# Kernel optimization log

Hardware: AMD Instinct MI355X
Metric: run time of the kernel (lower is better)

Reference implementation:

```python
import jax, jax.numpy as jnp
import numpy as np

CS = [32, 32, 64, 128, 256, 256, 128, 96, 96]
NC = 19
N0, N1, N2, N3, N4 = 50000, 20000, 8000, 3200, 1300


def build_shapes():
    cs = CS
    def rb(ci, co):
        t = [(27, ci, co), (27, co, co)]
        if ci != co:
            t.append((ci, co))  # 1x1 shortcut conv
        return t
    s = [(27, 4, cs[0]), (27, cs[0], cs[0])]                       # stem
    s += [(8, cs[0], cs[0])] + rb(cs[0], cs[1]) + rb(cs[1], cs[1])  # stage1
    s += [(8, cs[1], cs[1])] + rb(cs[1], cs[2]) + rb(cs[2], cs[2])  # stage2
    s += [(8, cs[2], cs[2])] + rb(cs[2], cs[3]) + rb(cs[3], cs[3])  # stage3
    s += [(8, cs[3], cs[3])] + rb(cs[3], cs[4]) + rb(cs[4], cs[4])  # stage4
    s += [(8, cs[4], cs[5])] + rb(cs[5] + cs[3], cs[5]) + rb(cs[5], cs[5])  # up1
    s += [(8, cs[5], cs[6])] + rb(cs[6] + cs[2], cs[6]) + rb(cs[6], cs[6])  # up2
    s += [(8, cs[6], cs[7])] + rb(cs[7] + cs[1], cs[7]) + rb(cs[7], cs[7])  # up3
    s += [(8, cs[7], cs[8])] + rb(cs[8] + cs[0], cs[8]) + rb(cs[8], cs[8])  # up4
    s += [(cs[8], NC), (NC,), (cs[8], cs[8]), (cs[8],), (cs[8], 128), (128,)]
    return s

P_TOTAL = sum(int(np.prod(sh)) for sh in build_shapes())


def _bn(x):
    # train-mode BatchNorm, gamma=1 beta=0 (set by weight_initialization)
    return (x - x.mean(0)) * jax.lax.rsqrt(jnp.var(x, 0) + 1e-5)


def _spconv(x, nbr, W):
    # sparse conv as gather-GEMM-scatter over K kernel offsets.
    # x: [Nin, Cin], nbr: [Nout, K] row indices into x, W: [K, Cin, Cout]
    acc0 = jnp.zeros((nbr.shape[0], W.shape[-1]), x.dtype)
    def step(acc, kw):
        idx, Wk = kw
        return acc + x[idx] @ Wk, None
    acc, _ = jax.lax.scan(step, acc0, (nbr.T, W))
    return acc


def _spdeconv(x, parent, off, W):
    # transposed ks=2 stride=2 conv: each fine voxel has exactly one coarse
    # parent and one kernel-offset id. out[i] = x[parent[i]] @ W[off[i]]
    y = jnp.einsum('nc,kcd->nkd', x[parent], W)  # [Nf, 8, Cout]
    return jnp.take_along_axis(y, off[:, None, None], axis=1)[:, 0, :]


def _cbr(x, nbr, W):
    return jax.nn.relu(_bn(_spconv(x, nbr, W)))


def _resblock(x, nbr, take, ci, co):
    w1 = take(); w2 = take()
    h = _bn(_spconv(jax.nn.relu(_bn(_spconv(x, nbr, w1))), nbr, w2))
    s = x if ci == co else _bn(x @ take())
    return jax.nn.relu(h + s)


def _forward(x, nbr0, nbr1, nbr2, nbr3, nbr4, d1, d2, d3, d4,
             u1p, u1o, u2p, u2o, u3p, u3o, u4p, u4o, params):
    parts = []
    o = 0
    for sh in build_shapes():
        n = int(np.prod(sh))
        parts.append(params[o:o + n].reshape(sh))
        o += n
    it = iter(parts)
    take = lambda: next(it)
    cs = CS
    x0 = _cbr(x, nbr0, take()); x0 = _cbr(x0, nbr0, take())            # stem
    h = _cbr(x0, d1, take())
    h = _resblock(h, nbr1, take, cs[0], cs[1]); x1 = _resblock(h, nbr1, take, cs[1], cs[1])
    h = _cbr(x1, d2, take())
    h = _resblock(h, nbr2, take, cs[1], cs[2]); x2 = _resblock(h, nbr2, take, cs[2], cs[2])
    h = _cbr(x2, d3, take())
    h = _resblock(h, nbr3, take, cs[2], cs[3]); x3 = _resblock(h, nbr3, take, cs[3], cs[3])
    h = _cbr(x3, d4, take())
    h = _resblock(h, nbr4, take, cs[3], cs[4]); x4 = _resblock(h, nbr4, take, cs[4], cs[4])
    y = jax.nn.relu(_bn(_spdeconv(x4, u1p, u1o, take())))
    y = jnp.concatenate([y, x3], 1)
    y = _resblock(y, nbr3, take, cs[5] + cs[3], cs[5]); y = _resblock(y, nbr3, take, cs[5], cs[5])
    y = jax.nn.relu(_bn(_spdeconv(y, u2p, u2o, take())))
    y = jnp.concatenate([y, x2], 1)
    y = _resblock(y, nbr2, take, cs[6] + cs[2], cs[6]); y = _resblock(y, nbr2, take, cs[6], cs[6])
    y = jax.nn.relu(_bn(_spdeconv(y, u3p, u3o, take())))
    y = jnp.concatenate([y, x1], 1)
    y = _resblock(y, nbr1, take, cs[7] + cs[1], cs[7]); y = _resblock(y, nbr1, take, cs[7], cs[7])
    y = jax.nn.relu(_bn(_spdeconv(y, u4p, u4o, take())))
    y = jnp.concatenate([y, x0], 1)
    y = _resblock(y, nbr0, take, cs[8] + cs[0], cs[8]); y = _resblock(y, nbr0, take, cs[8], cs[8])
    wc = take(); bc = take(); w1 = take(); b1 = take(); w2 = take(); b2 = take()
    out = y @ wc + bc                             # classifier logits [N0, NC]
    feat = jax.nn.relu(y @ w1 + b1) @ w2 + b2     # projection head [N0, 128]
    return out, feat


def setup_inputs() -> dict:
    key = jax.random.key(0)
    ks = jax.random.split(key, 20)
    ri = lambda k, shape, hi: jax.random.randint(k, shape, 0, hi, dtype=jnp.int32)
    return {
        'x': jax.random.normal(ks[0], (N0, 4), jnp.float32),
        'nbr0': ri(ks[1], (N0, 27), N0), 'nbr1': ri(ks[2], (N1, 27), N1),
        'nbr2': ri(ks[3], (N2, 27), N2), 'nbr3': ri(ks[4], (N3, 27), N3),
        'nbr4': ri(ks[5], (N4, 27), N4),
        'd1': ri(ks[6], (N1, 8), N0), 'd2': ri(ks[7], (N2, 8), N1),
        'd3': ri(ks[8], (N3, 8), N2), 'd4': ri(ks[9], (N4, 8), N3),
        'u1p': ri(ks[10], (N3,), N4), 'u1o': ri(ks[11], (N3,), 8),
        'u2p': ri(ks[12], (N2,), N3), 'u2o': ri(ks[13], (N2,), 8),
        'u3p': ri(ks[14], (N1,), N2), 'u3o': ri(ks[15], (N1,), 8),
        'u4p': ri(ks[16], (N0,), N1), 'u4o': ri(ks[17], (N0,), 8),
        'params': jax.random.normal(ks[18], (P_TOTAL,), jnp.float32) * 0.05,
    }


def reference(x, nbr0, nbr1, nbr2, nbr3, nbr4, d1, d2, d3, d4,
              u1p, u1o, u2p, u2o, u3p, u3o, u4p, u4o, params):
    return _forward(x, nbr0, nbr1, nbr2, nbr3, nbr4, d1, d2, d3, d4,
                    u1p, u1o, u2p, u2o, u3p, u3o, u4p, u4o, params)
```

## Files before the change

kernel.cpp:

```cpp
#include <hip/hip_runtime.h>
#include <hip/hip_bf16.h>
#include <stdint.h>

typedef __hip_bfloat16 hbf;
typedef unsigned short u16;
typedef __attribute__((ext_vector_type(8))) short bfrag;
typedef __attribute__((ext_vector_type(4))) float f4;

#define NP0 50000
#define NP1 20000
#define NP2 8000
#define NP3 3200
#define NP4 1300

static inline int cdiv(int a, int b) { return (a + b - 1) / b; }

static __device__ __forceinline__ float u2f(u16 u) { return __uint_as_float(((unsigned)u) << 16); }
static __device__ __forceinline__ u16 f2u(float f) {
  hbf h = __float2bfloat16(f);
  u16 r; __builtin_memcpy(&r, &h, 2); return r;
}
static __device__ __forceinline__ float pload(const void* P, int isbf, size_t i) {
  return isbf ? u2f(((const u16*)P)[i]) : ((const float*)P)[i];
}

__global__ void k_sniff(const void* __restrict__ xraw, int* __restrict__ flagp) {
  __shared__ float smax[256];
  const u16* u = (const u16*)xraw;
  float m = 0.f;
  for (int i = threadIdx.x; i < 2048; i += 256) {
    float v = u2f(u[2 * i]);
    if (isnan(v) || isinf(v)) m = 1e30f; else m = fmaxf(m, fabsf(v));
  }
  smax[threadIdx.x] = m;
  __syncthreads();
  for (int s = 128; s > 0; s >>= 1) {
    if (threadIdx.x < s) smax[threadIdx.x] = fmaxf(smax[threadIdx.x], smax[threadIdx.x + s]);
    __syncthreads();
  }
  if (threadIdx.x == 0) *flagp = (smax[0] < 1e4f) ? 1 : 0;
}

__global__ __launch_bounds__(256) void k_prep_frag(
    const void* __restrict__ P, const int* __restrict__ flagp, u16* __restrict__ W,
    long src, long halfel, int K, int CI, int CO, int CB32, int NT16)
{
  int f = *flagp;
  long total = (long)K * CB32 * NT16 * 64;
  for (long c = (long)blockIdx.x * 256 + threadIdx.x; c < total; c += (long)gridDim.x * 256) {
    int lane = (int)(c & 63); long t = c >> 6;
    int nt = (int)(t % NT16); t /= NT16;
    int cb = (int)(t % CB32); int k = (int)(t / CB32);
    int co = nt * 16 + (lane & 15);
    int cib = cb * 32 + (lane >> 4) * 8;
    u16 hi[8], lo[8];
#pragma unroll
    for (int j = 0; j < 8; ++j) {
      int ci = cib + j; float v = 0.f;
      if (ci < CI && co < CO) v = pload(P, f, src + ((size_t)k * CI + ci) * CO + co);
      u16 h = f2u(v);
      hi[j] = h;
      lo[j] = f2u(v - u2f(h));
    }
    *(bfrag*)(W + c * 8) = *(const bfrag*)hi;
    *(bfrag*)(W + halfel + c * 8) = *(const bfrag*)lo;
  }
}

__global__ void k_prep_bias(const void* __restrict__ P, const int* __restrict__ flagp,
                            float* __restrict__ B, long src, int n)
{
  int f = *flagp;
  int i = blockIdx.x * 256 + threadIdx.x;
  if (i < n) B[i] = pload(P, f, src + i);
}

__global__ void k_pad(const void* __restrict__ xraw, const int* __restrict__ flagp,
                      float* __restrict__ Xp, int N)
{
  int f = *flagp; int total = N * 32;
  for (int i = blockIdx.x * 256 + threadIdx.x; i < total; i += gridDim.x * 256) {
    int n = i >> 5, cc = i & 31;
    Xp[i] = (cc < 4) ? pload(xraw, f, (size_t)n * 4 + cc) : 0.f;
  }
}

template<int NT>
__global__ __launch_bounds__(256) void k_conv_mfma(
    const float* __restrict__ X, const int* __restrict__ nbr,
    const u16* __restrict__ Wp, long halfel, float* __restrict__ Y,
    const float* __restrict__ bias, int relu,
    int N, int K, int CB32, int NT16, int CO, int XS, int tlen, int atomic)
{
  const int lane = threadIdx.x & 63;
  const int wv = threadIdx.x >> 6;
  const int rowbase = blockIdx.x * 128 + wv * 32;
  const int ntb = blockIdx.y * NT;
  const int ml = lane & 15;
  const int quad = lane >> 4;
  const int ktot = K * CB32;
  const int t0 = blockIdx.z * tlen;
  const int t1 = (t0 + tlen < ktot) ? (t0 + tlen) : ktot;

  f4 acc[2][NT];
#pragma unroll
  for (int i = 0; i < 2; ++i)
#pragma unroll
    for (int j = 0; j < NT; ++j) acc[i][j] = (f4)(0.f);

  int k = t0 / CB32;
  int cb = t0 - k * CB32;
  int idx[2];
  bool fresh = true;

  for (int t = t0; t < t1; ++t) {
    if (fresh) {
#pragma unroll
      for (int mt = 0; mt < 2; ++mt) {
        int r = rowbase + mt * 16 + ml;
        idx[mt] = (r < N) ? (nbr ? nbr[(size_t)r * K + k] : r) : 0;
      }
      fresh = false;
    }
    const u16* WH = Wp + (size_t)t * NT16 * 512;
    const u16* WL = WH + halfel;
    bfrag bh[NT], bl[NT];
#pragma unroll
    for (int nt = 0; nt < NT; ++nt) {
      size_t o = ((size_t)(ntb + nt) * 64 + lane) * 8;
      bh[nt] = *(const bfrag*)(WH + o);
      bl[nt] = *(const bfrag*)(WL + o);
    }
    bfrag ahi[2], alo[2];
#pragma unroll
    for (int mt = 0; mt < 2; ++mt) {
      const float* ap = X + (size_t)idx[mt] * XS + cb * 32 + quad * 8;
      float4 q0 = *(const float4*)ap;
      float4 q1 = *(const float4*)(ap + 4);
      float av[8] = {q0.x, q0.y, q0.z, q0.w, q1.x, q1.y, q1.z, q1.w};
      u16 hi8[8], lo8[8];
#pragma unroll
      for (int j = 0; j < 8; ++j) {
        u16 hh = f2u(av[j]);
        hi8[j] = hh;
        lo8[j] = f2u(av[j] - u2f(hh));
      }
      __builtin_memcpy(&ahi[mt], hi8, 16);
      __builtin_memcpy(&alo[mt], lo8, 16);
    }
#pragma unroll
    for (int mt = 0; mt < 2; ++mt)
#pragma unroll
      for (int nt = 0; nt < NT; ++nt) {
        acc[mt][nt] = __builtin_amdgcn_mfma_f32_16x16x32_bf16(alo[mt], bh[nt], acc[mt][nt], 0, 0, 0);
        acc[mt][nt] = __builtin_amdgcn_mfma_f32_16x16x32_bf16(ahi[mt], bl[nt], acc[mt][nt], 0, 0, 0);
        acc[mt][nt] = __builtin_amdgcn_mfma_f32_16x16x32_bf16(ahi[mt], bh[nt], acc[mt][nt], 0, 0, 0);
      }
    if (++cb == CB32) { cb = 0; ++k; fresh = true; }
  }

#pragma unroll
  for (int mt = 0; mt < 2; ++mt) {
#pragma unroll
    for (int nt = 0; nt < NT; ++nt) {
      int col = (ntb + nt) * 16 + ml;
      if (col >= CO) continue;
      float bvv = bias ? bias[col] : 0.f;
#pragma unroll
      for (int reg = 0; reg < 4; ++reg) {
        int row = rowbase + mt * 16 + quad * 4 + reg;
        if (row < N) {
          if (atomic) {
            atomicAdd(&Y[(size_t)row * CO + col], acc[mt][nt][reg]);
          } else {
            float v = acc[mt][nt][reg] + bvv;
            if (relu) v = fmaxf(v, 0.f);
            Y[(size_t)row * CO + col] = v;
          }
        }
      }
    }
  }
}

__global__ void k_bias_relu(float* __restrict__ Y, const float* __restrict__ bias,
                            int relu, int total, int CO)
{
  int stride = gridDim.x * 256;
  for (int i = blockIdx.x * 256 + threadIdx.x; i < total; i += stride) {
    int c = i % CO;
    float v = Y[i] + (bias ? bias[c] : 0.f);
    if (relu) v = fmaxf(v, 0.f);
    Y[i] = v;
  }
}

static void launch_conv(hipStream_t s, int bx, const float* X, const int* nbr,
                        const u16* W, long halfel, float* Y, const float* bias, int relu,
                        int N, int K, int CB32, int NT16, int CO, int XS)
{
  int NT = (NT16 % 6 == 0) ? 6 : ((NT16 % 4 == 0) ? 4 : 2);
  int ny = NT16 / NT;
  int ktot = K * CB32;
  long blocks = (long)bx * ny;
  int ZS = 1;
  if (ktot > 1) {
    ZS = (int)((1024 + blocks - 1) / blocks);
    if (ZS > ktot) ZS = ktot;
    if (ZS < 1) ZS = 1;
  }
  int tlen = cdiv(ktot, ZS);
  ZS = cdiv(ktot, tlen);
  int atomic = (ZS > 1) ? 1 : 0;
  if (atomic) hipMemsetAsync(Y, 0, (size_t)N * CO * 4, s);
  dim3 g(bx, ny, ZS);
  if (NT == 6)      k_conv_mfma<6><<<g, 256, 0, s>>>(X, nbr, W, halfel, Y, bias, relu, N, K, CB32, NT16, CO, XS, tlen, atomic);
  else if (NT == 4) k_conv_mfma<4><<<g, 256, 0, s>>>(X, nbr, W, halfel, Y, bias, relu, N, K, CB32, NT16, CO, XS, tlen, atomic);
  else              k_conv_mfma<2><<<g, 256, 0, s>>>(X, nbr, W, halfel, Y, bias, relu, N, K, CB32, NT16, CO, XS, tlen, atomic);
  if (atomic && (bias || relu)) {
    int total = N * CO;
    int nb = cdiv(total, 1024); if (nb > 1024) nb = 1024; if (nb < 1) nb = 1;
    k_bias_relu<<<nb, 256, 0, s>>>(Y, bias, relu, total, CO);
  }
}

__global__ __launch_bounds__(256) void k_deconv(
    const float* __restrict__ X, const int* __restrict__ par, const int* __restrict__ off,
    const void* __restrict__ P, long wofs, const int* __restrict__ flagp,
    float* __restrict__ Y, int N, int CI, int CO)
{
  int f = *flagp;
  int lane = threadIdx.x & 63, wv = threadIdx.x >> 6;
  int n = blockIdx.y * 4 + wv; if (n >= N) return;
  int co = blockIdx.x * 64 + lane; if (co >= CO) return;
  const float* xr = X + (size_t)par[n] * CI;
  size_t wbase = wofs + (size_t)off[n] * CI * CO + co;
  float acc = 0.f;
  for (int ci = 0; ci < CI; ci += 4) {
    float4 xv = *(const float4*)(xr + ci);
    acc += xv.x * pload(P, f, wbase + (size_t)ci * CO);
    acc += xv.y * pload(P, f, wbase + (size_t)(ci + 1) * CO);
    acc += xv.z * pload(P, f, wbase + (size_t)(ci + 2) * CO);
    acc += xv.w * pload(P, f, wbase + (size_t)(ci + 3) * CO);
  }
  Y[(size_t)n * CO + co] = acc;
}

__global__ __launch_bounds__(256) void k_bn_stats(
    const float* __restrict__ X, float* __restrict__ st, int total, int C)
{
  __shared__ float ssum[384], ssq[384];
  for (int c = threadIdx.x; c < C; c += 256) { ssum[c] = 0.f; ssq[c] = 0.f; }
  __syncthreads();
  int gid = blockIdx.x * 256 + threadIdx.x;
  int total4 = total >> 2;
  int stride = gridDim.x * 256;
  int c0 = (gid * 4) % C;
  float s0 = 0.f, s1 = 0.f, s2 = 0.f, s3 = 0.f;
  float q0 = 0.f, q1 = 0.f, q2 = 0.f, q3 = 0.f;
  for (int i = gid; i < total4; i += stride) {
    float4 v = ((const float4*)X)[i];
    s0 += v.x; q0 += v.x * v.x;
    s1 += v.y; q1 += v.y * v.y;
    s2 += v.z; q2 += v.z * v.z;
    s3 += v.w; q3 += v.w * v.w;
  }
  atomicAdd(&ssum[c0], s0);     atomicAdd(&ssq[c0], q0);
  atomicAdd(&ssum[c0 + 1], s1); atomicAdd(&ssq[c0 + 1], q1);
  atomicAdd(&ssum[c0 + 2], s2); atomicAdd(&ssq[c0 + 2], q2);
  atomicAdd(&ssum[c0 + 3], s3); atomicAdd(&ssq[c0 + 3], q3);
  __syncthreads();
  for (int c = threadIdx.x; c < C; c += 256) {
    atomicAdd(&st[c], ssum[c]); atomicAdd(&st[384 + c], ssq[c]);
  }
}

__global__ __launch_bounds__(256) void k_bn_apply(
    const float* __restrict__ X, const float* __restrict__ st, const float* __restrict__ add,
    float* __restrict__ Y, int relu, int total, int C, float invN)
{
  __shared__ float mean[384], rsig[384];
  for (int c = threadIdx.x; c < C; c += 256) {
    float mm = st[c] * invN;
    float vv = st[384 + c] * invN - mm * mm;
    mean[c] = mm; rsig[c] = rsqrtf(vv + 1e-5f);
  }
  __syncthreads();
  int gid = blockIdx.x * 256 + threadIdx.x;
  int total4 = total >> 2;
  int stride = gridDim.x * 256;
  int c0 = (gid * 4) % C;
  float m0 = mean[c0], m1 = mean[c0 + 1], m2 = mean[c0 + 2], m3 = mean[c0 + 3];
  float r0 = rsig[c0], r1 = rsig[c0 + 1], r2 = rsig[c0 + 2], r3 = rsig[c0 + 3];
  for (int i = gid; i < total4; i += stride) {
    float4 v = ((const float4*)X)[i];
    v.x = (v.x - m0) * r0; v.y = (v.y - m1) * r1;
    v.z = (v.z - m2) * r2; v.w = (v.w - m3) * r3;
    if (add) {
      float4 a = ((const float4*)add)[i];
      v.x += a.x; v.y += a.y; v.z += a.z; v.w += a.w;
    }
    if (relu) {
      v.x = fmaxf(v.x, 0.f); v.y = fmaxf(v.y, 0.f);
      v.z = fmaxf(v.z, 0.f); v.w = fmaxf(v.w, 0.f);
    }
    ((float4*)Y)[i] = v;
  }
}

__global__ void k_copycols(const float* __restrict__ S, float* __restrict__ D,
                           int N, int Cs, int Cd, int off)
{
  int csq = Cs >> 2;
  int total4 = N * csq;
  int stride = gridDim.x * 256;
  for (int i = blockIdx.x * 256 + threadIdx.x; i < total4; i += stride) {
    int n = i / csq, cc = i - n * csq;
    ((float4*)D)[((size_t)n * Cd + off) / 4 + cc] = ((const float4*)S)[i];
  }
}

__global__ void k_store_dyn(const float* __restrict__ S, void* __restrict__ D,
                            const int* __restrict__ flagp, size_t eofs, int n)
{
  int f = *flagp;
  int n4 = n >> 2;
  int stride = gridDim.x * 256;
  for (int i = blockIdx.x * 256 + threadIdx.x; i < n4; i += stride) {
    float4 v = ((const float4*)S)[i];
    if (f) {
      ushort4 u;
      u.x = f2u(v.x); u.y = f2u(v.y); u.z = f2u(v.z); u.w = f2u(v.w);
      *(ushort4*)((u16*)D + eofs + (size_t)i * 4) = u;
    } else {
      *(float4*)((float*)D + eofs + (size_t)i * 4) = v;
    }
  }
}


extern "C" void kernel_launch(void* const* d_in, const int* in_sizes, int n_in,
                              void* d_out, int out_size, void* d_ws, size_t ws_size,
                              hipStream_t stream)
{
  const void* xraw = d_in[0];
  const int* nbr0 = (const int*)d_in[1];
  const int* nbr1 = (const int*)d_in[2];
  const int* nbr2 = (const int*)d_in[3];
  const int* nbr3 = (const int*)d_in[4];
  const int* nbr4 = (const int*)d_in[5];
  const int* d1 = (const int*)d_in[6];
  const int* d2 = (const int*)d_in[7];
  const int* d3 = (const int*)d_in[8];
  const int* d4 = (const int*)d_in[9];
  const int* u1p = (const int*)d_in[10]; const int* u1o = (const int*)d_in[11];
  const int* u2p = (const int*)d_in[12]; const int* u2o = (const int*)d_in[13];
  const int* u3p = (const int*)d_in[14]; const int* u3o = (const int*)d_in[15];
  const int* u4p = (const int*)d_in[16]; const int* u4o = (const int*)d_in[17];
  const void* params = d_in[18];
  (void)in_sizes; (void)n_in;

  char* base = (char*)d_ws; size_t off = 0;
  auto ab = [&](size_t bytes) -> void* { void* p = base + off; off += (bytes + 63) & ~(size_t)63; return p; };
  int* flagp = (int*)ab(64);
  float* st = (float*)ab((size_t)64 * 768 * 4);
  u16* Wst = (u16*)ab((size_t)5400000 * 2);
  float* Bstf = (float*)ab((size_t)512 * 4);
  float* x0 = (float*)ab((size_t)NP0 * 32 * 4);
  float* x1 = (float*)ab((size_t)NP1 * 32 * 4);
  float* x2 = (float*)ab((size_t)NP2 * 64 * 4);
  float* x3 = (float*)ab((size_t)NP3 * 128 * 4);
  float* x4 = (float*)ab((size_t)NP4 * 256 * 4);
  float* U  = (float*)ab((size_t)NP0 * 96 * 4);
  float* A  = (float*)ab((size_t)NP0 * 96 * 4);
  float* B  = (float*)ab((size_t)NP0 * 128 * 4);
  float* Xp = B;
  if (off > ws_size) { hipMemsetAsync(d_out, 0, (size_t)out_size * 2, stream); return; }

  long po = 0;
  int bnc = 0;

  auto prepF = [&](int K, int CI, int CO, int CB32, int NT16) -> long {
    long chunks = (long)K * CB32 * NT16 * 64;
    long halfel = chunks * 8;
    int nb = (int)((chunks + 255) / 256); if (nb > 4096) nb = 4096; if (nb < 1) nb = 1;
    k_prep_frag<<<nb, 256, 0, stream>>>(params, flagp, Wst, po, halfel, K, CI, CO, CB32, NT16);
    po += (long)K * CI * CO;
    return halfel;
  };
  auto convop = [&](const float* X, const int* nb_, int K, int CI, int CO, float* Y, int N, int XS) {
    int CB32 = cdiv(CI, 32), NT16 = cdiv(CO, 16);
    long halfel = prepF(K, CI, CO, CB32, NT16);
    launch_conv(stream, cdiv(N, 128), X, nb_, Wst, halfel, Y, nullptr, 0, N, K, CB32, NT16, CO, XS);
  };
  auto linop = [&](const float* X, int CI, int CO, float* Y, int N, bool bias, int relu) {
    int CB32 = cdiv(CI, 32), NT16 = cdiv(CO, 16);
    long halfel = prepF(1, CI, CO, CB32, NT16);
    const float* bp = nullptr;
    if (bias) {
      k_prep_bias<<<cdiv(CO, 256), 256, 0, stream>>>(params, flagp, Bstf, po, CO);
      po += CO; bp = Bstf;
    }
    launch_conv(stream, cdiv(N, 128), X, nullptr, Wst, halfel, Y, bp, relu, N, 1, CB32, NT16, CO, CI);
  };
  auto deconvop = [&](const float* X, const int* par, const int* ofv, int CI, int CO, float* Y, int N) {
    long wofs = po; po += (long)8 * CI * CO;
    dim3 g(cdiv(CO, 64), cdiv(N, 4));
    k_deconv<<<g, 256, 0, stream>>>(X, par, ofv, params, wofs, flagp, Y, N, CI, CO);
  };
  auto bnop = [&](const float* X, int N, int C, const float* add, int relu, float* out) {
    float* slot = st + (size_t)(bnc++) * 768;
    int total = N * C;
    int total4 = total >> 2;
    int nb1 = cdiv(total4, 4096); if (nb1 > 504) nb1 = 504; if (nb1 < 3) nb1 = 3;
    nb1 = ((nb1 + 2) / 3) * 3;
    k_bn_stats<<<nb1, 256, 0, stream>>>(X, slot, total, C);
    int nb2 = cdiv(total4, 2048); if (nb2 > 510) nb2 = 510; if (nb2 < 3) nb2 = 3;
    nb2 = ((nb2 + 2) / 3) * 3;
    k_bn_apply<<<nb2, 256, 0, stream>>>(X, slot, add, out ? out : (float*)X, relu, total, C, 1.0f / (float)N);
  };
  auto copyop = [&](const float* S, float* D, int N, int Cs, int Cd, int o2) {
    int total4 = (N * Cs) >> 2;
    int nb3 = cdiv(total4, 1024); if (nb3 > 1024) nb3 = 1024; if (nb3 < 1) nb3 = 1;
    k_copycols<<<nb3, 256, 0, stream>>>(S, D, N, Cs, Cd, o2);
  };
  auto storeop = [&](const float* S, size_t eo, int n) {
    int nb4 = cdiv(n >> 2, 1024); if (nb4 > 1024) nb4 = 1024; if (nb4 < 1) nb4 = 1;
    k_store_dyn<<<nb4, 256, 0, stream>>>(S, d_out, flagp, eo, n);
  };
  auto resblock = [&](const int* nb, int N, int CI, int CO,
                      float* H, float* t1, float* t2, float* OUT) {
    convop(H, nb, 27, CI, CO, t1, N, CI);
    bnop(t1, N, CO, nullptr, 1, nullptr);
    convop(t1, nb, 27, CO, CO, t2, N, CO);
    const float* S;
    if (CI == CO) S = H;
    else { linop(H, CI, CO, t1, N, false, 0); bnop(t1, N, CO, nullptr, 0, nullptr); S = t1; }
    bnop(t2, N, CO, S, 1, OUT);
  };

  k_sniff<<<1, 256, 0, stream>>>(xraw, flagp);
  hipMemsetAsync(st, 0, (size_t)64 * 768 * 4, stream);
  k_pad<<<1024, 256, 0, stream>>>(xraw, flagp, Xp, NP0);

  convop(Xp, nbr0, 27, 4, 32, A, NP0, 32);  bnop(A, NP0, 32, nullptr, 1, nullptr);
  convop(A, nbr0, 27, 32, 32, x0, NP0, 32); bnop(x0, NP0, 32, nullptr, 1, nullptr);
  convop(x0, d1, 8, 32, 32, U, NP1, 32); bnop(U, NP1, 32, nullptr, 1, nullptr);
  resblock(nbr1, NP1, 32, 32, U, A, B, U);
  resblock(nbr1, NP1, 32, 32, U, A, B, x1);
  convop(x1, d2, 8, 32, 32, U, NP2, 32); bnop(U, NP2, 32, nullptr, 1, nullptr);
  resblock(nbr2, NP2, 32, 64, U, A, B, U);
  resblock(nbr2, NP2, 64, 64, U, A, B, x2);
  convop(x2, d3, 8, 64, 64, U, NP3, 64); bnop(U, NP3, 64, nullptr, 1, nullptr);
  resblock(nbr3, NP3, 64, 128, U, A, B, U);
  resblock(nbr3, NP3, 128, 128, U, A, B, x3);
  convop(x3, d4, 8, 128, 128, U, NP4, 128); bnop(U, NP4, 128, nullptr, 1, nullptr);
  resblock(nbr4, NP4, 128, 256, U, A, B, U);
  resblock(nbr4, NP4, 256, 256, U, A, B, x4);
  deconvop(x4, u1p, u1o, 256, 256, A, NP3); bnop(A, NP3, 256, nullptr, 1, nullptr);
  copyop(A, B, NP3, 256, 384, 0); copyop(x3, B, NP3, 128, 384, 256);
  resblock(nbr3, NP3, 384, 256, B, A, U, B);
  resblock(nbr3, NP3, 256, 256, B, A, U, U);
  deconvop(U, u2p, u2o, 256, 128, A, NP2); bnop(A, NP2, 128, nullptr, 1, nullptr);
  copyop(A, B, NP2, 128, 192, 0); copyop(x2, B, NP2, 64, 192, 128);
  resblock(nbr2, NP2, 192, 128, B, A, U, B);
  resblock(nbr2, NP2, 128, 128, B, A, U, U);
  deconvop(U, u3p, u3o, 128, 96, A, NP1); bnop(A, NP1, 96, nullptr, 1, nullptr);
  copyop(A, B, NP1, 96, 128, 0); copyop(x1, B, NP1, 32, 128, 96);
  resblock(nbr1, NP1, 128, 96, B, A, U, B);
  resblock(nbr1, NP1, 96, 96, B, A, U, U);
  deconvop(U, u4p, u4o, 96, 96, A, NP0); bnop(A, NP0, 96, nullptr, 1, nullptr);
  copyop(A, B, NP0, 96, 128, 0); copyop(x0, B, NP0, 32, 128, 96);
  resblock(nbr0, NP0, 128, 96, B, A, U, B);
  resblock(nbr0, NP0, 96, 96, B, A, U, U);
  linop(U, 96, 19, x0, NP0, true, 0);
  linop(U, 96, 96, A, NP0, true, 1);
  linop(A, 96, 128, B, NP0, true, 0);
  storeop(x0, 0, NP0 * 19);
  storeop(B, (size_t)NP0 * 19, NP0 * 128);
}
```

Measured before the change: 4.423 ms.

## Batch all weight fragment preparation into one kernel and skip low-half MFMA for bf16 params

Weight splitting for every conv layer is replaced by a single k_prep_all launch driven by a host-built descriptor table, writing all layers into one large workspace buffer when space allows. This removes many small per-layer prep launches. The conv kernel also reads the dtype flag, and when parameters are bf16 (low half zero) it drops the bl loads and the ahi*bl MFMA, cutting MFMA work by a third. It adds a host-to-device table copy and relies on the hand-written table matching the forward layer order.

```diff
diff --git a/kernel.cpp b/kernel.cpp
--- a/kernel.cpp
+++ b/kernel.cpp
@@ -23,6 +23,14 @@
 static __device__ __forceinline__ float pload(const void* P, int isbf, size_t i) {
   return isbf ? u2f(((const u16*)P)[i]) : ((const float*)P)[i];
 }
+
+
+struct PrepD {
+  long cpre;
+  long src;
+  long dst;
+  int K, CI, CO, CB32, NT16, pad;
+};
 
 __global__ void k_sniff(const void* __restrict__ xraw, int* __restrict__ flagp) {
   __shared__ float smax[256];
@@ -39,6 +47,35 @@
     __syncthreads();
   }
   if (threadIdx.x == 0) *flagp = (smax[0] < 1e4f) ? 1 : 0;
+}
+
+__global__ __launch_bounds__(256) void k_prep_all(
+    const void* __restrict__ P, const int* __restrict__ flagp, u16* __restrict__ W,
+    const PrepD* __restrict__ T, int NL, long totalC, long totalE)
+{
+  int f = *flagp;
+  int L = 0;
+  for (long c = (long)blockIdx.x * 256 + threadIdx.x; c < totalC; c += (long)gridDim.x * 256) {
+    while (L + 1 < NL && c >= T[L + 1].cpre) ++L;
+    PrepD d = T[L];
+    long lc = c - d.cpre;
+    int lane = (int)(lc & 63); long t = lc >> 6;
+    int nt = (int)(t % d.NT16); t /= d.NT16;
+    int cb = (int)(t % d.CB32); int k = (int)(t / d.CB32);
+    int co = nt * 16 + (lane & 15);
+    int cib = cb * 32 + (lane >> 4) * 8;
+    u16 hi[8], lo[8];
+#pragma unroll
+    for (int j = 0; j < 8; ++j) {
+      int ci = cib + j; float v = 0.f;
+      if (ci < d.CI && co < d.CO) v = pload(P, f, d.src + ((size_t)k * d.CI + ci) * d.CO + co);
+      u16 h = f2u(v);
+      hi[j] = h;
+      lo[j] = f2u(v - u2f(h));
+    }
+    *(bfrag*)(W + d.dst + lc * 8) = *(const bfrag*)hi;
+    *(bfrag*)(W + totalE + d.dst + lc * 8) = *(const bfrag*)lo;
+  }
 }
 
 __global__ __launch_bounds__(256) void k_prep_frag(
@@ -89,9 +126,10 @@
 __global__ __launch_bounds__(256) void k_conv_mfma(
     const float* __restrict__ X, const int* __restrict__ nbr,
     const u16* __restrict__ Wp, long halfel, float* __restrict__ Y,
-    const float* __restrict__ bias, int relu,
+    const float* __restrict__ bias, int relu, const int* __restrict__ flagp,
     int N, int K, int CB32, int NT16, int CO, int XS, int tlen, int atomic)
 {
+  const int f = *flagp;
   const int lane = threadIdx.x & 63;
   const int wv = threadIdx.x >> 6;
   const int rowbase = blockIdx.x * 128 + wv * 32;
@@ -113,50 +151,95 @@
   int idx[2];
   bool fresh = true;
 
-  for (int t = t0; t < t1; ++t) {
-    if (fresh) {
+  if (f) {
+    for (int t = t0; t < t1; ++t) {
+      if (fresh) {
+#pragma unroll
+        for (int mt = 0; mt < 2; ++mt) {
+          int r = rowbase + mt * 16 + ml;
+          idx[mt] = (r < N) ? (nbr ? nbr[(size_t)r * K + k] : r) : 0;
+        }
+        fresh = false;
+      }
+      const u16* WH = Wp + (size_t)t * NT16 * 512;
+      bfrag bh[NT];
+#pragma unroll
+      for (int nt = 0; nt < NT; ++nt) {
+        size_t o = ((size_t)(ntb + nt) * 64 + lane) * 8;
+        bh[nt] = *(const bfrag*)(WH + o);
+      }
+      bfrag ahi[2], alo[2];
 #pragma unroll
       for (int mt = 0; mt < 2; ++mt) {
-        int r = rowbase + mt * 16 + ml;
-        idx[mt] = (r < N) ? (nbr ? nbr[(size_t)r * K + k] : r) : 0;
+        const float* ap = X + (size_t)idx[mt] * XS + cb * 32 + quad * 8;
+        float4 q0 = *(const float4*)ap;
+        float4 q1 = *(const float4*)(ap + 4);
+        float av[8] = {q0.x, q0.y, q0.z, q0.w, q1.x, q1.y, q1.z, q1.w};
+        u16 hi8[8], lo8[8];
+#pragma unroll
+        for (int j = 0; j < 8; ++j) {
+          u16 hh = f2u(av[j]);
+          hi8[j] = hh;
+          lo8[j] = f2u(av[j] - u2f(hh));
+        }
+        __builtin_memcpy(&ahi[mt], hi8, 16);
+        __builtin_memcpy(&alo[mt], lo8, 16);
       }
-      fresh = false;
-    }
-    const u16* WH = Wp + (size_t)t * NT16 * 512;
-    const u16* WL = WH + halfel;
-    bfrag bh[NT], bl[NT];
-#pragma unroll
-    for (int nt = 0; nt < NT; ++nt) {
-      size_t o = ((size_t)(ntb + nt) * 64 + lane) * 8;
-      bh[nt] = *(const bfrag*)(WH + o);
-      bl[nt] = *(const bfrag*)(WL + o);
-    }
-    bfrag ahi[2], alo[2];
-#pragma unroll
-    for (int mt = 0; mt < 2; ++mt) {
-      const float* ap = X + (size_t)idx[mt] * XS + cb * 32 + quad * 8;
-      float4 q0 = *(const float4*)ap;
-      float4 q1 = *(const float4*)(ap + 4);
-      float av[8] = {q0.x, q0.y, q0.z, q0.w, q1.x, q1.y, q1.z, q1.w};
-      u16 hi8[8], lo8[8];
-#pragma unroll
-      for (int j = 0; j < 8; ++j) {
-        u16 hh = f2u(av[j]);
-        hi8[j] = hh;
-        lo8[j] = f2u(av[j] - u2f(hh));
+#pragma unroll
+      for (int mt = 0; mt < 2; ++mt)
+#pragma unroll
+        for (int nt = 0; nt < NT; ++nt) {
+          acc[mt][nt] = __builtin_amdgcn_mfma_f32_16x16x32_bf16(alo[mt], bh[nt], acc[mt][nt], 0, 0, 0);
+          acc[mt][nt] = __builtin_amdgcn_mfma_f32_16x16x32_bf16(ahi[mt], bh[nt], acc[mt][nt], 0, 0, 0);
+        }
+      if (++cb == CB32) { cb = 0; ++k; fresh = true; }
+    }
+  } else {
+    for (int t = t0; t < t1; ++t) {
+      if (fresh) {
+#pragma unroll
+        for (int mt = 0; mt < 2; ++mt) {
+          int r = rowbase + mt * 16 + ml;
+          idx[mt] = (r < N) ? (nbr ? nbr[(size_t)r * K + k] : r) : 0;
+        }
+        fresh = false;
       }
-      __builtin_memcpy(&ahi[mt], hi8, 16);
-      __builtin_memcpy(&alo[mt], lo8, 16);
-    }
-#pragma unroll
-    for (int mt = 0; mt < 2; ++mt)
+      const u16* WH = Wp + (size_t)t * NT16 * 512;
+      const u16* WL = WH + halfel;
+      bfrag bh[NT], bl[NT];
 #pragma unroll
       for (int nt = 0; nt < NT; ++nt) {
-        acc[mt][nt] = __builtin_amdgcn_mfma_f32_16x16x32_bf16(alo[mt], bh[nt], acc[mt][nt], 0, 0, 0);
-        acc[mt][nt] = __builtin_amdgcn_mfma_f32_16x16x32_bf16(ahi[mt], bl[nt], acc[mt][nt], 0, 0, 0);
-        acc[mt][nt] = __builtin_amdgcn_mfma_f32_16x16x32_bf16(ahi[mt], bh[nt], acc[mt][nt], 0, 0, 0);
+        size_t o = ((size_t)(ntb + nt) * 64 + lane) * 8;
+        bh[nt] = *(const bfrag*)(WH + o);
+        bl[nt] = *(const bfrag*)(WL + o);
       }
-    if (++cb == CB32) { cb = 0; ++k; fresh = true; }
+      bfrag ahi[2], alo[2];
+#pragma unroll
+      for (int mt = 0; mt < 2; ++mt) {
+        const float* ap = X + (size_t)idx[mt] * XS + cb * 32 + quad * 8;
+        float4 q0 = *(const float4*)ap;
+        float4 q1 = *(const float4*)(ap + 4);
+        float av[8] = {q0.x, q0.y, q0.z, q0.w, q1.x, q1.y, q1.z, q1.w};
+        u16 hi8[8], lo8[8];
+#pragma unroll
+        for (int j = 0; j < 8; ++j) {
+          u16 hh = f2u(av[j]);
+          hi8[j] = hh;
+          lo8[j] = f2u(av[j] - u2f(hh));
+        }
+        __builtin_memcpy(&ahi[mt], hi8, 16);
+        __builtin_memcpy(&alo[mt], lo8, 16);
+      }
+#pragma unroll
+      for (int mt = 0; mt < 2; ++mt)
+#pragma unroll
+        for (int nt = 0; nt < NT; ++nt) {
+          acc[mt][nt] = __builtin_amdgcn_mfma_f32_16x16x32_bf16(alo[mt], bh[nt], acc[mt][nt], 0, 0, 0);
+          acc[mt][nt] = __builtin_amdgcn_mfma_f32_16x16x32_bf16(ahi[mt], bl[nt], acc[mt][nt], 0, 0, 0);
+          acc[mt][nt] = __builtin_amdgcn_mfma_f32_16x16x32_bf16(ahi[mt], bh[nt], acc[mt][nt], 0, 0, 0);
+        }
+      if (++cb == CB32) { cb = 0; ++k; fresh = true; }
+    }
   }
 
 #pragma unroll
@@ -197,7 +280,7 @@
 
 static void launch_conv(hipStream_t s, int bx, const float* X, const int* nbr,
                         const u16* W, long halfel, float* Y, const float* bias, int relu,
-                        int N, int K, int CB32, int NT16, int CO, int XS)
+                        const int* flagp, int N, int K, int CB32, int NT16, int CO, int XS)
 {
   int NT = (NT16 % 6 == 0) ? 6 : ((NT16 % 4 == 0) ? 4 : 2);
   int ny = NT16 / NT;
@@ -214,9 +297,9 @@
   int atomic = (ZS > 1) ? 1 : 0;
   if (atomic) hipMemsetAsync(Y, 0, (size_t)N * CO * 4, s);
   dim3 g(bx, ny, ZS);
-  if (NT == 6)      k_conv_mfma<6><<<g, 256, 0, s>>>(X, nbr, W, halfel, Y, bias, relu, N, K, CB32, NT16, CO, XS, tlen, atomic);
-  else if (NT == 4) k_conv_mfma<4><<<g, 256, 0, s>>>(X, nbr, W, halfel, Y, bias, relu, N, K, CB32, NT16, CO, XS, tlen, atomic);
-  else              k_conv_mfma<2><<<g, 256, 0, s>>>(X, nbr, W, halfel, Y, bias, relu, N, K, CB32, NT16, CO, XS, tlen, atomic);
+  if (NT == 6)      k_conv_mfma<6><<<g, 256, 0, s>>>(X, nbr, W, halfel, Y, bias, relu, flagp, N, K, CB32, NT16, CO, XS, tlen, atomic);
+  else if (NT == 4) k_conv_mfma<4><<<g, 256, 0, s>>>(X, nbr, W, halfel, Y, bias, relu, flagp, N, K, CB32, NT16, CO, XS, tlen, atomic);
+  else              k_conv_mfma<2><<<g, 256, 0, s>>>(X, nbr, W, halfel, Y, bias, relu, flagp, N, K, CB32, NT16, CO, XS, tlen, atomic);
   if (atomic && (bias || relu)) {
     int total = N * CO;
     int nb = cdiv(total, 1024); if (nb > 1024) nb = 1024; if (nb < 1) nb = 1;
@@ -336,6 +419,34 @@
       *(float4*)((float*)D + eofs + (size_t)i * 4) = v;
     }
   }
+}
+
+static int build_table(PrepD* T, long* totalC, long* totalE) {
+  int n = 0; long po = 0, ce = 0, cc = 0;
+  auto W = [&](int K, int CI, int CO) {
+    int CB = cdiv(CI, 32), NTx = cdiv(CO, 16);
+    long ch = (long)K * CB * NTx * 64;
+    T[n].cpre = cc; T[n].src = po; T[n].dst = ce;
+    T[n].K = K; T[n].CI = CI; T[n].CO = CO; T[n].CB32 = CB; T[n].NT16 = NTx; T[n].pad = 0;
+    ++n; cc += ch; ce += ch * 8; po += (long)K * CI * CO;
+  };
+  auto SKIP = [&](long e) { po += e; };
+  W(27, 4, 32); W(27, 32, 32);
+  W(8, 32, 32); W(27, 32, 32); W(27, 32, 32); W(27, 32, 32); W(27, 32, 32);
+  W(8, 32, 32); W(27, 32, 64); W(27, 64, 64); W(1, 32, 64); W(27, 64, 64); W(27, 64, 64);
+  W(8, 64, 64); W(27, 64, 128); W(27, 128, 128); W(1, 64, 128); W(27, 128, 128); W(27, 128, 128);
+  W(8, 128, 128); W(27, 128, 256); W(27, 256, 256); W(1, 128, 256); W(27, 256, 256); W(27, 256, 256);
+  SKIP(8L * 256 * 256);
+  W(27, 384, 256); W(27, 256, 256); W(1, 384, 256); W(27, 256, 256); W(27, 256, 256);
+  SKIP(8L * 256 * 128);
+  W(27, 192, 128); W(27, 128, 128); W(1, 192, 128); W(27, 128, 128); W(27, 128, 128);
+  SKIP(8L * 128 * 96);
+  W(27, 128, 96); W(27, 96, 96); W(1, 128, 96); W(27, 96, 96); W(27, 96, 96);
+  SKIP(8L * 96 * 96);
+  W(27, 128, 96); W(27, 96, 96); W(1, 128, 96); W(27, 96, 96); W(27, 96, 96);
+  W(1, 96, 19); SKIP(19); W(1, 96, 96); SKIP(96); W(1, 96, 128); SKIP(128);
+  *totalC = cc; *totalE = ce;
+  return n;
 }
 
 
@@ -360,11 +471,14 @@
   const void* params = d_in[18];
   (void)in_sizes; (void)n_in;
 
+  static PrepD h_table[64];
+  long totalC = 0, totalE = 0;
+  int NL = build_table(h_table, &totalC, &totalE);
+
   char* base = (char*)d_ws; size_t off = 0;
   auto ab = [&](size_t bytes) -> void* { void* p = base + off; off += (bytes + 63) & ~(size_t)63; return p; };
   int* flagp = (int*)ab(64);
   float* st = (float*)ab((size_t)64 * 768 * 4);
-  u16* Wst = (u16*)ab((size_t)5400000 * 2);
   float* Bstf = (float*)ab((size_t)512 * 4);
   float* x0 = (float*)ab((size_t)NP0 * 32 * 4);
   float* x1 = (float*)ab((size_t)NP1 * 32 * 4);
@@ -375,10 +489,22 @@
   float* A  = (float*)ab((size_t)NP0 * 96 * 4);
   float* B  = (float*)ab((size_t)NP0 * 128 * 4);
   float* Xp = B;
+
+  size_t wall_bytes = (size_t)totalE * 4;
+  size_t rem = (ws_size > off) ? (ws_size - off) : 0;
+  bool bigprep = rem >= wall_bytes + 8192;
+  u16* Wall = nullptr; PrepD* d_table = nullptr; u16* Wst = nullptr;
+  if (bigprep) {
+    Wall = (u16*)ab(wall_bytes);
+    d_table = (PrepD*)ab(4096);
+  } else {
+    Wst = (u16*)ab((size_t)5400000 * 2);
+  }
   if (off > ws_size) { hipMemsetAsync(d_out, 0, (size_t)out_size * 2, stream); return; }
 
   long po = 0;
   int bnc = 0;
+  int wli = 0;
 
   auto prepF = [&](int K, int CI, int CO, int CB32, int NT16) -> long {
     long chunks = (long)K * CB32 * NT16 * 64;
@@ -388,20 +514,30 @@
     po += (long)K * CI * CO;
     return halfel;
   };
+  auto getW = [&](int K, int CI, int CO, int CB32, int NT16, const u16** Wp, long* he) {
+    if (bigprep) {
+      *Wp = Wall + h_table[wli].dst; *he = totalE;
+      ++wli; po += (long)K * CI * CO;
+    } else {
+      *he = prepF(K, CI, CO, CB32, NT16); *Wp = Wst;
+    }
+  };
   auto convop = [&](const float* X, const int* nb_, int K, int CI, int CO, float* Y, int N, int XS) {
     int CB32 = cdiv(CI, 32), NT16 = cdiv(CO, 16);
-    long halfel = prepF(K, CI, CO, CB32, NT16);
-    launch_conv(stream, cdiv(N, 128), X, nb_, Wst, halfel, Y, nullptr, 0, N, K, CB32, NT16, CO, XS);
+    const u16* Wp; long he;
+    getW(K, CI, CO, CB32, NT16, &Wp, &he);
+    launch_conv(stream, cdiv(N, 128), X, nb_, Wp, he, Y, nullptr, 0, flagp, N, K, CB32, NT16, CO, XS);
   };
   auto linop = [&](const float* X, int CI, int CO, float* Y, int N, bool bias, int relu) {
     int CB32 = cdiv(CI, 32), NT16 = cdiv(CO, 16);
-    long halfel = prepF(1, CI, CO, CB32, NT16);
+    const u16* Wp; long he;
+    getW(1, CI, CO, CB32, NT16, &Wp, &he);
     const float* bp = nullptr;
     if (bias) {
       k_prep_bias<<<cdiv(CO, 256), 256, 0, stream>>>(params, flagp, Bstf, po, CO);
       po += CO; bp = Bstf;
     }
-    launch_conv(stream, cdiv(N, 128), X, nullptr, Wst, halfel, Y, bp, relu, N, 1, CB32, NT16, CO, CI);
+    launch_conv(stream, cdiv(N, 128), X, nullptr, Wp, he, Y, bp, relu, flagp, N, 1, CB32, NT16, CO, CI);
   };
   auto deconvop = [&](const float* X, const int* par, const int* ofv, int CI, int CO, float* Y, int N) {
     long wofs = po; po += (long)8 * CI * CO;
@@ -440,6 +576,11 @@
   };
 
   k_sniff<<<1, 256, 0, stream>>>(xraw, flagp);
+  if (bigprep) {
+    hipMemcpyAsync(d_table, h_table, (size_t)NL * sizeof(PrepD), hipMemcpyHostToDevice, stream);
+    int nbp = (int)((totalC + 255) / 256); if (nbp > 4096) nbp = 4096;
+    k_prep_all<<<nbp, 256, 0, stream>>>(params, flagp, Wall, d_table, NL, totalC, totalE);
+  }
   hipMemsetAsync(st, 0, (size_t)64 * 768 * 4, stream);
   k_pad<<<1024, 256, 0, stream>>>(xraw, flagp, Xp, NP0);
 
```

Result: faster. 4.298 ms (-2.8%).
